# Optimization experiments

Measured on AMD Instinct MI355X. Metric: run time of the kernel, lower is better.

The kernel has to match this reference:

```python
import jax, jax.numpy as jnp
import numpy as np

D_MODEL = 1024
N_HEADS = 16
HEAD_DIM = D_MODEL // N_HEADS


def setup_inputs() -> dict:
    key = jax.random.key(0)
    ks = jax.random.split(key, 5)
    B, S = 4, 2048
    scale = 1.0 / np.sqrt(D_MODEL)
    return {
        "x": jax.random.normal(ks[0], (B, S, D_MODEL), dtype=jnp.float32),
        "W_q": jax.random.normal(ks[1], (D_MODEL, D_MODEL), dtype=jnp.float32) * scale,
        "W_k": jax.random.normal(ks[2], (D_MODEL, D_MODEL), dtype=jnp.float32) * scale,
        "W_v": jax.random.normal(ks[3], (D_MODEL, D_MODEL), dtype=jnp.float32) * scale,
        "W_o": jax.random.normal(ks[4], (D_MODEL, D_MODEL), dtype=jnp.float32) * scale,
    }


def reference(x, W_q, W_k, W_v, W_o):
    B, S, _ = x.shape
    # nn.Linear(d,d,bias=False): y = x @ W.T ; W stored as (out,in)
    def proj(W):
        y = jnp.einsum('bsd,ed->bse', x, W)
        return y.reshape(B, S, N_HEADS, HEAD_DIM).transpose(0, 2, 1, 3)  # (B,H,S,Dh)
    q, k, v = proj(W_q), proj(W_k), proj(W_v)
    scores = jnp.einsum('bhqd,bhkd->bhqk', q, k) / np.sqrt(HEAD_DIM)
    causal = jnp.tril(jnp.ones((S, S), dtype=bool))  # (S,S)
    scores = jnp.where(causal[None, None], scores, -jnp.inf)
    attn = jax.nn.softmax(scores, axis=-1)
    heads = jnp.einsum('bhqk,bhkd->bhqd', attn, v)
    concat = heads.transpose(0, 2, 1, 3).reshape(B, S, D_MODEL)
    return jnp.einsum('bsd,ed->bse', concat, W_o)
```

## Files before the change

kernel.cpp:

```cpp
#include <hip/hip_runtime.h>
#include <hip/hip_bf16.h>

#define D_MODEL 1024
#define N_HEADS 16
#define HEAD_DIM 64
#define BATCH 4
#define SEQ 2048
#define M_ROWS (BATCH * SEQ)

typedef __attribute__((ext_vector_type(8))) __bf16 bf16x8;
typedef __attribute__((ext_vector_type(8))) short short8;
typedef __attribute__((ext_vector_type(4))) float f32x4;

static __device__ __forceinline__ unsigned short f2bf_rne(float f) {
  unsigned int u = __float_as_uint(f);
  u += 0x7FFFu + ((u >> 16) & 1u);
  return (unsigned short)(u >> 16);
}

#if __has_builtin(__builtin_amdgcn_exp2f)
#define EXP2F(x) __builtin_amdgcn_exp2f(x)
#else
#define EXP2F(x) exp2f(x)
#endif

static __device__ __forceinline__ void gl_lds16(const unsigned short* g, unsigned short* l) {
  __builtin_amdgcn_global_load_lds((const __attribute__((address_space(1))) unsigned int*)g,
                                   (__attribute__((address_space(3))) unsigned int*)l, 16, 0, 0);
}

__global__ __launch_bounds__(256) void cvt_all(const float* __restrict__ x,
                                               const float* __restrict__ wq,
                                               const float* __restrict__ wk,
                                               const float* __restrict__ wv,
                                               const float* __restrict__ wo,
                                               unsigned short* __restrict__ xb,
                                               unsigned short* __restrict__ wqb,
                                               unsigned short* __restrict__ wkb,
                                               unsigned short* __restrict__ wvb,
                                               unsigned short* __restrict__ wob) {
  const int bid = blockIdx.x;
  const float* src;
  unsigned short* dst;
  int i;
  if (bid < 8192) {
    src = x; dst = xb; i = bid * 256 + threadIdx.x;
  } else {
    int r = bid - 8192;
    int w = r >> 10;
    i = (r & 1023) * 256 + threadIdx.x;
    switch (w) {
      case 0: src = wq; dst = wqb; break;
      case 1: src = wk; dst = wkb; break;
      case 2: src = wv; dst = wvb; break;
      default: src = wo; dst = wob; break;
    }
  }
  float4 f = reinterpret_cast<const float4*>(src)[i];
  ushort4 o;
  o.x = f2bf_rne(f.x); o.y = f2bf_rne(f.y); o.z = f2bf_rne(f.z); o.w = f2bf_rne(f.w);
  reinterpret_cast<ushort4*>(dst)[i] = o;
}

__global__ __launch_bounds__(256) void qkv_gemm(const unsigned short* __restrict__ A,
                                                const unsigned short* __restrict__ Wq,
                                                const unsigned short* __restrict__ Wk,
                                                const unsigned short* __restrict__ Wv,
                                                unsigned short* __restrict__ Qo,
                                                unsigned short* __restrict__ Ko,
                                                unsigned short* __restrict__ Vt) {
  __shared__ __align__(16) unsigned short smem[16384];
  const int t = threadIdx.x;
  const int widx = blockIdx.x >> 3;
  const int bn = blockIdx.x & 7, bm = blockIdx.y;
  const unsigned short* Bw = (widx == 0) ? Wq : (widx == 1) ? Wk : Wv;
  const float oscale = (widx == 0) ? 0.18033688f : 1.0f;
  const int K = D_MODEL, N = D_MODEL;

  const int wave = t >> 6, lane = t & 63;
  const int wm = (wave >> 1) * 64, wn = (wave & 1) * 64;
  const int lr = lane & 15, quad = lane >> 4;

  const int g0 = wave * 128 + lane, g1 = g0 + 64;
  const int r0 = g0 >> 2, c0 = (g0 & 3) << 3;
  const int r1 = g1 >> 2, c1 = (g1 & 3) << 3;
  const unsigned short* Arow0 = A + (size_t)(bm * 128 + r0) * K + c0;
  const unsigned short* Arow1 = A + (size_t)(bm * 128 + r1) * K + c1;
  const unsigned short* Brow0 = Bw + (size_t)(bn * 128 + r0) * K + c0;
  const unsigned short* Brow1 = Bw + (size_t)(bn * 128 + r1) * K + c1;

  f32x4 acc[4][4] = {};

  gl_lds16(Arow0, &smem[g0 * 8]);
  gl_lds16(Arow1, &smem[g1 * 8]);
  gl_lds16(Brow0, &smem[4096 + g0 * 8]);
  gl_lds16(Brow1, &smem[4096 + g1 * 8]);
  __syncthreads();

  for (int it = 0; it < 32; it++) {
    const int cur = (it & 1) * 8192;
    if (it + 1 < 32) {
      const int nxt = 8192 - cur;
      const int k1 = (it + 1) * 32;
      gl_lds16(Arow0 + k1, &smem[nxt + g0 * 8]);
      gl_lds16(Arow1 + k1, &smem[nxt + g1 * 8]);
      gl_lds16(Brow0 + k1, &smem[nxt + 4096 + g0 * 8]);
      gl_lds16(Brow1 + k1, &smem[nxt + 4096 + g1 * 8]);
    }
    const unsigned short* As = &smem[cur];
    const unsigned short* Bs = &smem[cur + 4096];

    bf16x8 af[4], bfr[4];
#pragma unroll
    for (int mt = 0; mt < 4; mt++)
      af[mt] = __builtin_bit_cast(
          bf16x8, *reinterpret_cast<const short8*>(&As[(wm + mt * 16 + lr) * 32 + quad * 8]));
#pragma unroll
    for (int nt = 0; nt < 4; nt++)
      bfr[nt] = __builtin_bit_cast(
          bf16x8, *reinterpret_cast<const short8*>(&Bs[(wn + nt * 16 + lr) * 32 + quad * 8]));
#pragma unroll
    for (int mt = 0; mt < 4; mt++)
#pragma unroll
      for (int nt = 0; nt < 4; nt++)
        acc[mt][nt] = __builtin_amdgcn_mfma_f32_16x16x32_bf16(af[mt], bfr[nt], acc[mt][nt], 0, 0, 0);
    __syncthreads();
  }

  if (widx < 2) {
    unsigned short* Cp = (widx == 0) ? Qo : Ko;
#pragma unroll
    for (int mt = 0; mt < 4; mt++) {
#pragma unroll
      for (int nt = 0; nt < 4; nt++) {
        int col = bn * 128 + wn + nt * 16 + lr;
#pragma unroll
        for (int r = 0; r < 4; r++) {
          int row = bm * 128 + wm + mt * 16 + quad * 4 + r;
          Cp[(size_t)row * N + col] = f2bf_rne(acc[mt][nt][r] * oscale);
        }
      }
    }
  } else {
    const int b = bm >> 4;
    const int s0 = (bm & 15) * 128;
#pragma unroll
    for (int half = 0; half < 2; half++) {
      __syncthreads();
      if ((wave & 1) == half) {
#pragma unroll
        for (int nt = 0; nt < 4; nt++) {
#pragma unroll
          for (int mt = 0; mt < 4; mt++) {
#pragma unroll
            for (int r = 0; r < 4; r++) {
              int cl = nt * 16 + lr;
              int rl = wm + mt * 16 + quad * 4 + r;
              smem[cl * 136 + rl] = f2bf_rne(acc[mt][nt][r]);
            }
          }
        }
      }
      __syncthreads();
      const int h2 = bn * 2 + half;
      const size_t rowbase = ((size_t)(b * N_HEADS + h2)) * HEAD_DIM;
#pragma unroll
      for (int i = 0; i < 4; i++) {
        int c = i * 256 + t;
        int d = c >> 4, s8 = (c & 15) * 8;
        uint4 v = *reinterpret_cast<const uint4*>(&smem[d * 136 + s8]);
        *reinterpret_cast<uint4*>(Vt + (rowbase + d) * SEQ + s0 + s8) = v;
      }
    }
  }
}

__global__ __launch_bounds__(256) void gemm_bt_f32(const unsigned short* __restrict__ A,
                                                   const unsigned short* __restrict__ Bw,
                                                   float* __restrict__ Cp,
                                                   int M, int N, int K) {
  __shared__ __align__(16) unsigned short smem[12288];
  const int t = threadIdx.x;
  const int bn = blockIdx.x, bm = blockIdx.y;
  const int wave = t >> 6, lane = t & 63;
  const int wm = (wave >> 1) * 64, wn = (wave & 1) * 32;
  const int lr = lane & 15, quad = lane >> 4;

  const int g0 = t, g1 = t + 256;
  const int ar0 = g0 >> 2, ac0 = (g0 & 3) << 3;
  const int ar1 = g1 >> 2, ac1 = (g1 & 3) << 3;
  const int br = t >> 2, bc = (t & 3) << 3;
  const unsigned short* Arow0 = A + (size_t)(bm * 128 + ar0) * K + ac0;
  const unsigned short* Arow1 = A + (size_t)(bm * 128 + ar1) * K + ac1;
  const unsigned short* Brow = Bw + (size_t)(bn * 64 + br) * K + bc;

  f32x4 acc[4][2] = {};

  gl_lds16(Arow0, &smem[g0 * 8]);
  gl_lds16(Arow1, &smem[g1 * 8]);
  gl_lds16(Brow, &smem[4096 + t * 8]);
  __syncthreads();

  const int niter = K / 32;
  for (int it = 0; it < niter; it++) {
    const int cur = (it & 1) * 6144;
    if (it + 1 < niter) {
      const int nxt = 6144 - cur;
      const int k1 = (it + 1) * 32;
      gl_lds16(Arow0 + k1, &smem[nxt + g0 * 8]);
      gl_lds16(Arow1 + k1, &smem[nxt + g1 * 8]);
      gl_lds16(Brow + k1, &smem[nxt + 4096 + t * 8]);
    }
    const unsigned short* As = &smem[cur];
    const unsigned short* Bs = &smem[cur + 4096];

    bf16x8 af[4], bfr[2];
#pragma unroll
    for (int mt = 0; mt < 4; mt++)
      af[mt] = __builtin_bit_cast(
          bf16x8, *reinterpret_cast<const short8*>(&As[(wm + mt * 16 + lr) * 32 + quad * 8]));
#pragma unroll
    for (int nt = 0; nt < 2; nt++)
      bfr[nt] = __builtin_bit_cast(
          bf16x8, *reinterpret_cast<const short8*>(&Bs[(wn + nt * 16 + lr) * 32 + quad * 8]));
#pragma unroll
    for (int mt = 0; mt < 4; mt++)
#pragma unroll
      for (int nt = 0; nt < 2; nt++)
        acc[mt][nt] = __builtin_amdgcn_mfma_f32_16x16x32_bf16(af[mt], bfr[nt], acc[mt][nt], 0, 0, 0);
    __syncthreads();
  }

#pragma unroll
  for (int mt = 0; mt < 4; mt++) {
#pragma unroll
    for (int nt = 0; nt < 2; nt++) {
      int col = bn * 64 + wn + nt * 16 + lr;
#pragma unroll
      for (int r = 0; r < 4; r++) {
        int row = bm * 128 + wm + mt * 16 + quad * 4 + r;
        Cp[(size_t)row * N + col] = acc[mt][nt][r];
      }
    }
  }
}

__global__ __launch_bounds__(512, 4) void attn_causal(const unsigned short* __restrict__ Q,
                                                      const unsigned short* __restrict__ Km,
                                                      const unsigned short* __restrict__ Vt,
                                                      unsigned short* __restrict__ O) {
  __shared__ __align__(16) unsigned short Ks[64 * 72];
  __shared__ __align__(16) unsigned short Vs[64 * 72];
  __shared__ __align__(16) unsigned short Ps[8][16 * 72];

  const int bid = blockIdx.x;
  const int p = bid & 7;
  const int h = (bid >> 3) & 15;
  const int b = bid >> 7;

  const int t = threadIdx.x;
  const int wave = t >> 6, lane = t & 63;
  const int lr = lane & 15, quad = lane >> 4;

  const size_t base = (size_t)b * SEQ * D_MODEL + h * HEAD_DIM;
  const unsigned short* Qb = Q + base;
  const unsigned short* Kb = Km + base;
  const unsigned short* Vb = Vt + (size_t)(b * N_HEADS + h) * HEAD_DIM * SEQ;
  unsigned short* pw = &Ps[wave][0];

  const int sr = t >> 3, sc = (t & 7) << 3;

  for (int ph = 0; ph < 2; ph++) {
    const int qt = ph ? (15 - p) : p;
    const int m0 = qt * 128 + wave * 16;
    const int ntiles = (qt + 1) * 2;

    bf16x8 qf[2];
#pragma unroll
    for (int kk = 0; kk < 2; kk++)
      qf[kk] = __builtin_bit_cast(
          bf16x8,
          *reinterpret_cast<const short8*>(Qb + (size_t)(m0 + lr) * D_MODEL + kk * 32 + quad * 8));

    f32x4 o_acc[4] = {};
    float lsum[4] = {};

    uint4 ra = *reinterpret_cast<const uint4*>(Kb + (size_t)sr * D_MODEL + sc);
    uint4 rc = *reinterpret_cast<const uint4*>(Vb + (size_t)sr * SEQ + sc);

    for (int kt = 0; kt < ntiles; kt++) {
      const int kv0 = kt * 64;
      __syncthreads();
      *reinterpret_cast<uint4*>(&Ks[sr * 72 + sc]) = ra;
      *reinterpret_cast<uint4*>(&Vs[sr * 72 + sc]) = rc;
      __syncthreads();
      if (kt + 1 < ntiles) {
        const int kv1 = kv0 + 64;
        ra = *reinterpret_cast<const uint4*>(Kb + (size_t)(kv1 + sr) * D_MODEL + sc);
        rc = *reinterpret_cast<const uint4*>(Vb + (size_t)sr * SEQ + kv1 + sc);
      }

      f32x4 sAcc[4] = {};
#pragma unroll
      for (int kk = 0; kk < 2; kk++) {
        bf16x8 kf[4];
#pragma unroll
        for (int j = 0; j < 4; j++)
          kf[j] = __builtin_bit_cast(
              bf16x8, *reinterpret_cast<const short8*>(&Ks[(j * 16 + lr) * 72 + kk * 32 + quad * 8]));
#pragma unroll
        for (int j = 0; j < 4; j++)
          sAcc[j] = __builtin_amdgcn_mfma_f32_16x16x32_bf16(qf[kk], kf[j], sAcc[j], 0, 0, 0);
      }

      asm volatile("s_waitcnt lgkmcnt(0)" ::: "memory");
      const bool needmask = (kv0 + 63 > m0);
#pragma unroll
      for (int r = 0; r < 4; r++) {
        const int qpos = m0 + quad * 4 + r;
        float e[4];
#pragma unroll
        for (int j = 0; j < 4; j++) e[j] = EXP2F(sAcc[j][r]);
        if (needmask) {
#pragma unroll
          for (int j = 0; j < 4; j++)
            if (kv0 + j * 16 + lr > qpos) e[j] = 0.f;
        }
        lsum[r] += (e[0] + e[1]) + (e[2] + e[3]);
        unsigned short* pr = &pw[(quad * 4 + r) * 72];
#pragma unroll
        for (int j = 0; j < 4; j++) pr[j * 16 + lr] = f2bf_rne(e[j]);
      }
      asm volatile("s_waitcnt lgkmcnt(0)" ::: "memory");

#pragma unroll
      for (int kk = 0; kk < 2; kk++) {
        bf16x8 pf = __builtin_bit_cast(
            bf16x8, *reinterpret_cast<const short8*>(&pw[lr * 72 + kk * 32 + quad * 8]));
#pragma unroll
        for (int c = 0; c < 4; c++) {
          bf16x8 vv = __builtin_bit_cast(
              bf16x8, *reinterpret_cast<const short8*>(&Vs[(c * 16 + lr) * 72 + kk * 32 + quad * 8]));
          o_acc[c] = __builtin_amdgcn_mfma_f32_16x16x32_bf16(pf, vv, o_acc[c], 0, 0, 0);
        }
      }
    }

#pragma unroll
    for (int r = 0; r < 4; r++) {
      float l = lsum[r];
#pragma unroll
      for (int off = 1; off < 16; off <<= 1) l += __shfl_xor(l, off, 64);
      const float inv = 1.f / l;
      const int qpos = m0 + quad * 4 + r;
#pragma unroll
      for (int c = 0; c < 4; c++)
        O[base + (size_t)qpos * D_MODEL + c * 16 + lr] = f2bf_rne(o_acc[c][r] * inv);
    }
  }
}

extern "C" void kernel_launch(void* const* d_in, const int* in_sizes, int n_in,
                              void* d_out, int out_size, void* d_ws, size_t ws_size,
                              hipStream_t stream) {
  const float* x  = (const float*)d_in[0];
  const float* Wq = (const float*)d_in[1];
  const float* Wk = (const float*)d_in[2];
  const float* Wv = (const float*)d_in[3];
  const float* Wo = (const float*)d_in[4];
  float* out = (float*)d_out;

  char* ws = (char*)d_ws;
  const size_t SZ_X = (size_t)M_ROWS * D_MODEL * 2;
  const size_t SZ_W = (size_t)D_MODEL * D_MODEL * 2;
  unsigned short* xb  = (unsigned short*)(ws);
  unsigned short* wqb = (unsigned short*)(ws + SZ_X);
  unsigned short* wkb = (unsigned short*)(ws + SZ_X + 1 * SZ_W);
  unsigned short* wvb = (unsigned short*)(ws + SZ_X + 2 * SZ_W);
  unsigned short* wob = (unsigned short*)(ws + SZ_X + 3 * SZ_W);
  unsigned short* Qb  = (unsigned short*)(ws + 1 * SZ_X + 4 * SZ_W);
  unsigned short* Kb  = (unsigned short*)(ws + 2 * SZ_X + 4 * SZ_W);
  unsigned short* Vt  = (unsigned short*)(ws + 3 * SZ_X + 4 * SZ_W);
  unsigned short* Ob  = xb;

  cvt_all<<<12288, 256, 0, stream>>>(x, Wq, Wk, Wv, Wo, xb, wqb, wkb, wvb, wob);

  qkv_gemm<<<dim3(24, 64), 256, 0, stream>>>(xb, wqb, wkb, wvb, Qb, Kb, Vt);

  attn_causal<<<512, 512, 0, stream>>>(Qb, Kb, Vt, Ob);

  gemm_bt_f32<<<dim3(16, 64), 256, 0, stream>>>(Ob, wob, out, M_ROWS, D_MODEL, D_MODEL);
}
```

Before: 265.4 us.

## Double query rows per wave in causal attention to reuse K/V tiles

Each wave now processes two 16-row query subtiles (256 query rows per block) against each shared K/V tile, halving the grid to 256 blocks. This halves K/V global and shared-memory traffic per query and gives more MFMA work per LDS read. In exchange it uses more registers and LDS for P, lowers the launch-bounds occupancy hint, and leaves fewer blocks to balance the causal workload.

```diff
diff --git a/kernel.cpp b/kernel.cpp
--- a/kernel.cpp
+++ b/kernel.cpp
@@ -245,18 +245,18 @@
   }
 }
 
-__global__ __launch_bounds__(512, 4) void attn_causal(const unsigned short* __restrict__ Q,
+__global__ __launch_bounds__(512, 2) void attn_causal(const unsigned short* __restrict__ Q,
                                                       const unsigned short* __restrict__ Km,
                                                       const unsigned short* __restrict__ Vt,
                                                       unsigned short* __restrict__ O) {
   __shared__ __align__(16) unsigned short Ks[64 * 72];
   __shared__ __align__(16) unsigned short Vs[64 * 72];
-  __shared__ __align__(16) unsigned short Ps[8][16 * 72];
+  __shared__ __align__(16) unsigned short Ps[8][32 * 72];
 
   const int bid = blockIdx.x;
-  const int p = bid & 7;
-  const int h = (bid >> 3) & 15;
-  const int b = bid >> 7;
+  const int p = bid & 3;
+  const int h = (bid >> 2) & 15;
+  const int b = bid >> 6;
 
   const int t = threadIdx.x;
   const int wave = t >> 6, lane = t & 63;
@@ -271,19 +271,21 @@
   const int sr = t >> 3, sc = (t & 7) << 3;
 
   for (int ph = 0; ph < 2; ph++) {
-    const int qt = ph ? (15 - p) : p;
-    const int m0 = qt * 128 + wave * 16;
-    const int ntiles = (qt + 1) * 2;
-
-    bf16x8 qf[2];
-#pragma unroll
-    for (int kk = 0; kk < 2; kk++)
-      qf[kk] = __builtin_bit_cast(
-          bf16x8,
-          *reinterpret_cast<const short8*>(Qb + (size_t)(m0 + lr) * D_MODEL + kk * 32 + quad * 8));
-
-    f32x4 o_acc[4] = {};
-    float lsum[4] = {};
+    const int qt = ph ? (7 - p) : p;
+    const int m0 = qt * 256 + wave * 32;
+    const int ntiles = (qt + 1) * 4;
+
+    bf16x8 qf[2][2];
+#pragma unroll
+    for (int s = 0; s < 2; s++)
+#pragma unroll
+      for (int kk = 0; kk < 2; kk++)
+        qf[s][kk] = __builtin_bit_cast(
+            bf16x8, *reinterpret_cast<const short8*>(
+                        Qb + (size_t)(m0 + s * 16 + lr) * D_MODEL + kk * 32 + quad * 8));
+
+    f32x4 o_acc[2][4] = {};
+    float lsum[2][4] = {};
 
     uint4 ra = *reinterpret_cast<const uint4*>(Kb + (size_t)sr * D_MODEL + sc);
     uint4 rc = *reinterpret_cast<const uint4*>(Vb + (size_t)sr * SEQ + sc);
@@ -300,7 +302,7 @@
         rc = *reinterpret_cast<const uint4*>(Vb + (size_t)sr * SEQ + kv1 + sc);
       }
 
-      f32x4 sAcc[4] = {};
+      f32x4 sAcc[2][4] = {};
 #pragma unroll
       for (int kk = 0; kk < 2; kk++) {
         bf16x8 kf[4];
@@ -309,53 +311,69 @@
           kf[j] = __builtin_bit_cast(
               bf16x8, *reinterpret_cast<const short8*>(&Ks[(j * 16 + lr) * 72 + kk * 32 + quad * 8]));
 #pragma unroll
-        for (int j = 0; j < 4; j++)
-          sAcc[j] = __builtin_amdgcn_mfma_f32_16x16x32_bf16(qf[kk], kf[j], sAcc[j], 0, 0, 0);
+        for (int s = 0; s < 2; s++)
+#pragma unroll
+          for (int j = 0; j < 4; j++)
+            sAcc[s][j] =
+                __builtin_amdgcn_mfma_f32_16x16x32_bf16(qf[s][kk], kf[j], sAcc[s][j], 0, 0, 0);
       }
 
       asm volatile("s_waitcnt lgkmcnt(0)" ::: "memory");
-      const bool needmask = (kv0 + 63 > m0);
-#pragma unroll
-      for (int r = 0; r < 4; r++) {
-        const int qpos = m0 + quad * 4 + r;
-        float e[4];
-#pragma unroll
-        for (int j = 0; j < 4; j++) e[j] = EXP2F(sAcc[j][r]);
-        if (needmask) {
-#pragma unroll
-          for (int j = 0; j < 4; j++)
-            if (kv0 + j * 16 + lr > qpos) e[j] = 0.f;
+#pragma unroll
+      for (int s = 0; s < 2; s++) {
+        const int msub = m0 + s * 16;
+        const bool needmask = (kv0 + 63 > msub);
+#pragma unroll
+        for (int r = 0; r < 4; r++) {
+          const int qpos = msub + quad * 4 + r;
+          float e[4];
+#pragma unroll
+          for (int j = 0; j < 4; j++) e[j] = EXP2F(sAcc[s][j][r]);
+          if (needmask) {
+#pragma unroll
+            for (int j = 0; j < 4; j++)
+              if (kv0 + j * 16 + lr > qpos) e[j] = 0.f;
+          }
+          lsum[s][r] += (e[0] + e[1]) + (e[2] + e[3]);
+          unsigned short* pr = &pw[(s * 16 + quad * 4 + r) * 72];
+#pragma unroll
+          for (int j = 0; j < 4; j++) pr[j * 16 + lr] = f2bf_rne(e[j]);
         }
-        lsum[r] += (e[0] + e[1]) + (e[2] + e[3]);
-        unsigned short* pr = &pw[(quad * 4 + r) * 72];
-#pragma unroll
-        for (int j = 0; j < 4; j++) pr[j * 16 + lr] = f2bf_rne(e[j]);
       }
       asm volatile("s_waitcnt lgkmcnt(0)" ::: "memory");
 
 #pragma unroll
       for (int kk = 0; kk < 2; kk++) {
-        bf16x8 pf = __builtin_bit_cast(
-            bf16x8, *reinterpret_cast<const short8*>(&pw[lr * 72 + kk * 32 + quad * 8]));
+        bf16x8 pf[2];
+#pragma unroll
+        for (int s = 0; s < 2; s++)
+          pf[s] = __builtin_bit_cast(
+              bf16x8,
+              *reinterpret_cast<const short8*>(&pw[(s * 16 + lr) * 72 + kk * 32 + quad * 8]));
 #pragma unroll
         for (int c = 0; c < 4; c++) {
           bf16x8 vv = __builtin_bit_cast(
               bf16x8, *reinterpret_cast<const short8*>(&Vs[(c * 16 + lr) * 72 + kk * 32 + quad * 8]));
-          o_acc[c] = __builtin_amdgcn_mfma_f32_16x16x32_bf16(pf, vv, o_acc[c], 0, 0, 0);
+#pragma unroll
+          for (int s = 0; s < 2; s++)
+            o_acc[s][c] = __builtin_amdgcn_mfma_f32_16x16x32_bf16(pf[s], vv, o_acc[s][c], 0, 0, 0);
         }
       }
     }
 
 #pragma unroll
-    for (int r = 0; r < 4; r++) {
-      float l = lsum[r];
-#pragma unroll
-      for (int off = 1; off < 16; off <<= 1) l += __shfl_xor(l, off, 64);
-      const float inv = 1.f / l;
-      const int qpos = m0 + quad * 4 + r;
-#pragma unroll
-      for (int c = 0; c < 4; c++)
-        O[base + (size_t)qpos * D_MODEL + c * 16 + lr] = f2bf_rne(o_acc[c][r] * inv);
+    for (int s = 0; s < 2; s++) {
+#pragma unroll
+      for (int r = 0; r < 4; r++) {
+        float l = lsum[s][r];
+#pragma unroll
+        for (int off = 1; off < 16; off <<= 1) l += __shfl_xor(l, off, 64);
+        const float inv = 1.f / l;
+        const int qpos = m0 + s * 16 + quad * 4 + r;
+#pragma unroll
+        for (int c = 0; c < 4; c++)
+          O[base + (size_t)qpos * D_MODEL + c * 16 + lr] = f2bf_rne(o_acc[s][c][r] * inv);
+      }
     }
   }
 }
@@ -387,7 +405,7 @@
 
   qkv_gemm<<<dim3(24, 64), 256, 0, stream>>>(xb, wqb, wkb, wvb, Qb, Kb, Vt);
 
-  attn_causal<<<512, 512, 0, stream>>>(Qb, Kb, Vt, Ob);
+  attn_causal<<<256, 512, 0, stream>>>(Qb, Kb, Vt, Ob);
 
   gemm_bt_f32<<<dim3(16, 64), 256, 0, stream>>>(Ob, wob, out, M_ROWS, D_MODEL, D_MODEL);
 }
```

New measurement: 269.4 us. No clear change (+1.5%).

## Double-buffer K/V tiles with direct global-to-LDS loads and XOR swizzle

Applied to the files above, without the earlier changes.

Attention K/V tiles now load straight from global memory into a two-stage LDS buffer with a direct-to-LDS helper, replacing the register staging and explicit LDS stores. This drops one of the two barriers per tile and lets the next tile's load overlap the current tile's MFMA work. The padded row stride of 72 becomes an unpadded stride of 64 with an XOR column swizzle to avoid bank conflicts. The trade-offs are twice the K/V LDS footprint, which may lower occupancy. Correctness also depends on the helper or the barrier waiting for outstanding vector-memory loads before the data is read.

```diff
diff --git a/kernel.cpp b/kernel.cpp
--- a/kernel.cpp
+++ b/kernel.cpp
@@ -249,8 +249,7 @@
                                                       const unsigned short* __restrict__ Km,
                                                       const unsigned short* __restrict__ Vt,
                                                       unsigned short* __restrict__ O) {
-  __shared__ __align__(16) unsigned short Ks[64 * 72];
-  __shared__ __align__(16) unsigned short Vs[64 * 72];
+  __shared__ __align__(16) unsigned short Kv[2][2][64 * 64];
   __shared__ __align__(16) unsigned short Ps[8][16 * 72];
 
   const int bid = blockIdx.x;
@@ -261,6 +260,7 @@
   const int t = threadIdx.x;
   const int wave = t >> 6, lane = t & 63;
   const int lr = lane & 15, quad = lane >> 4;
+  const int cxor = lr & 7;
 
   const size_t base = (size_t)b * SEQ * D_MODEL + h * HEAD_DIM;
   const unsigned short* Qb = Q + base;
@@ -268,7 +268,10 @@
   const unsigned short* Vb = Vt + (size_t)(b * N_HEADS + h) * HEAD_DIM * SEQ;
   unsigned short* pw = &Ps[wave][0];
 
-  const int sr = t >> 3, sc = (t & 7) << 3;
+  const int srow = t >> 3;
+  const int scol = ((t & 7) ^ (srow & 7)) << 3;
+  const unsigned short* Kg = Kb + (size_t)srow * D_MODEL + scol;
+  const unsigned short* Vg = Vb + (size_t)srow * SEQ + scol;
 
   for (int ph = 0; ph < 2; ph++) {
     const int qt = ph ? (15 - p) : p;
@@ -285,20 +288,19 @@
     f32x4 o_acc[4] = {};
     float lsum[4] = {};
 
-    uint4 ra = *reinterpret_cast<const uint4*>(Kb + (size_t)sr * D_MODEL + sc);
-    uint4 rc = *reinterpret_cast<const uint4*>(Vb + (size_t)sr * SEQ + sc);
+    gl_lds16(Kg, &Kv[0][0][t * 8]);
+    gl_lds16(Vg, &Kv[0][1][t * 8]);
 
     for (int kt = 0; kt < ntiles; kt++) {
+      const int cur = kt & 1;
       const int kv0 = kt * 64;
       __syncthreads();
-      *reinterpret_cast<uint4*>(&Ks[sr * 72 + sc]) = ra;
-      *reinterpret_cast<uint4*>(&Vs[sr * 72 + sc]) = rc;
-      __syncthreads();
       if (kt + 1 < ntiles) {
-        const int kv1 = kv0 + 64;
-        ra = *reinterpret_cast<const uint4*>(Kb + (size_t)(kv1 + sr) * D_MODEL + sc);
-        rc = *reinterpret_cast<const uint4*>(Vb + (size_t)sr * SEQ + kv1 + sc);
-      }
+        gl_lds16(Kg + (size_t)(kv0 + 64) * D_MODEL, &Kv[1 - cur][0][t * 8]);
+        gl_lds16(Vg + kv0 + 64, &Kv[1 - cur][1][t * 8]);
+      }
+      const unsigned short* Ks = &Kv[cur][0][0];
+      const unsigned short* Vs = &Kv[cur][1][0];
 
       f32x4 sAcc[4] = {};
 #pragma unroll
@@ -307,7 +309,8 @@
 #pragma unroll
         for (int j = 0; j < 4; j++)
           kf[j] = __builtin_bit_cast(
-              bf16x8, *reinterpret_cast<const short8*>(&Ks[(j * 16 + lr) * 72 + kk * 32 + quad * 8]));
+              bf16x8, *reinterpret_cast<const short8*>(
+                          &Ks[(j * 16 + lr) * 64 + ((kk * 4 + quad) ^ cxor) * 8]));
 #pragma unroll
         for (int j = 0; j < 4; j++)
           sAcc[j] = __builtin_amdgcn_mfma_f32_16x16x32_bf16(qf[kk], kf[j], sAcc[j], 0, 0, 0);
@@ -340,7 +343,8 @@
 #pragma unroll
         for (int c = 0; c < 4; c++) {
           bf16x8 vv = __builtin_bit_cast(
-              bf16x8, *reinterpret_cast<const short8*>(&Vs[(c * 16 + lr) * 72 + kk * 32 + quad * 8]));
+              bf16x8, *reinterpret_cast<const short8*>(
+                          &Vs[(c * 16 + lr) * 64 + ((kk * 4 + quad) ^ cxor) * 8]));
           o_acc[c] = __builtin_amdgcn_mfma_f32_16x16x32_bf16(pf, vv, o_acc[c], 0, 0, 0);
         }
       }
```

After: 262.1 us. About the same (-1.2%).
